# Performance work log

Measured on AMD Instinct MI355X. Metric: run time of the kernel, lower is better.

The kernel has to match this reference:

```python
import jax, jax.numpy as jnp
import numpy as np

J = 25
C_IN, HID, LAT = 3, 64, 32


def _graph_conv(x, A, W, b):
    # x: [N,T,J,Cin]; A: [J,J]; W: [Cin,Cout]; b: [Cout]
    A = jax.nn.softmax(A, axis=-1)
    # fused adjacency mix + projection: (A @ x) @ W + b
    x = jnp.einsum('ij,ntjc->ntic', A, x)
    return jnp.einsum('ntjc,cd->ntjd', x, W) + b


def setup_inputs() -> dict:
    key = jax.random.key(0)
    ks = jax.random.split(key, 13)
    x = jax.random.normal(ks[0], (32, 2048, J, C_IN), dtype=jnp.float32)
    eye = jnp.eye(J, dtype=jnp.float32)
    def lin(kw, kb, cin, cout):
        W = jax.random.normal(kw, (cin, cout), dtype=jnp.float32) / np.sqrt(cin)
        b = jax.random.normal(kb, (cout,), dtype=jnp.float32) * 0.01
        return W, b
    W1, b1 = lin(ks[1], ks[2], C_IN, HID)
    W2, b2 = lin(ks[3], ks[4], HID, LAT)
    W3, b3 = lin(ks[5], ks[6], LAT, HID)
    W4, b4 = lin(ks[7], ks[8], HID, C_IN)
    return {
        'x': x,
        'A1': eye, 'W1': W1, 'b1': b1,
        'A2': eye, 'W2': W2, 'b2': b2,
        'A3': eye, 'W3': W3, 'b3': b3,
        'A4': eye, 'W4': W4, 'b4': b4,
    }


def reference(x, A1, W1, b1, A2, W2, b2, A3, W3, b3, A4, W4, b4):
    h = jax.nn.relu(_graph_conv(x, A1, W1, b1))     # encoder_g1 + relu
    z = _graph_conv(h, A2, W2, b2)                  # encoder_g2 (no relu)
    h_dec = jax.nn.relu(_graph_conv(z, A3, W3, b3)) # decoder_g1 + relu
    out = _graph_conv(h_dec, A4, W4, b4)            # decoder_g2
    return out
```

## Files before the change

kernel.cpp:

```cpp
#include <hip/hip_runtime.h>
#include <math.h>

#define J 25
#define NJC 75
#define NWAVE 4
#define NTHREADS 256
#define NFPW 16

#define O_A1P  0
#define O_APP  1024
#define O_A4B  2048
#define O_W2T  3072
#define O_W3T  5120
#define O_W1A  7168
#define O_W4C  8192
#define O_B4   8512
#define O_BPPF 8576
#define CWS_SZ 8704

using bf16x2 = __attribute__((ext_vector_type(2))) __bf16;
using bf16x8 = __attribute__((ext_vector_type(8))) __bf16;
using f32x4  = __attribute__((ext_vector_type(4))) float;
using f32x16 = __attribute__((ext_vector_type(16))) float;

__device__ inline bf16x8 zero8() {
    bf16x8 z;
    #pragma unroll
    for (int j = 0; j < 8; j++) z[j] = (__bf16)0.f;
    return z;
}

#if defined(__has_builtin)
#if __has_builtin(__builtin_amdgcn_cvt_pk_bf16_f32)
#define HAVE_PK_BF16 1
#endif
#endif

__device__ inline bf16x2 cvt2(float a, float b) {
#ifdef HAVE_PK_BF16
    return __builtin_amdgcn_cvt_pk_bf16_f32(a, b);
#else
    bf16x2 r; r[0] = (__bf16)a; r[1] = (__bf16)b; return r;
#endif
}
__device__ inline bf16x8 pk8(const f32x16& acc, int st) {
    const int b = 8 * st;
    bf16x8 r;
    #pragma unroll
    for (int p = 0; p < 4; p++) {
        bf16x2 v = cvt2(acc[b + 2 * p], acc[b + 2 * p + 1]);
        r[2 * p] = v[0]; r[2 * p + 1] = v[1];
    }
    return r;
}

__global__ __launch_bounds__(NTHREADS, 2) void gcn_fused(
    const float* __restrict__ x,
    const float* __restrict__ A1, const float* __restrict__ W1, const float* __restrict__ b1,
    const float* __restrict__ A2, const float* __restrict__ W2, const float* __restrict__ b2,
    const float* __restrict__ A3, const float* __restrict__ W3, const float* __restrict__ b3,
    const float* __restrict__ A4, const float* __restrict__ W4, const float* __restrict__ b4,
    float* __restrict__ out)
{
    __shared__ __align__(16) float  TS[3189];
    __shared__ __align__(16) __bf16 CWS[CWS_SZ];

    const int t = threadIdx.x;

    {
        float* T   = TS;
        float* bpp = T + 3125;
        float* T0 = T;        float* T1 = T + 625;  float* T2 = T + 1250;
        float* T3 = T + 1875; float* T4 = T + 2500;

        if (t < 100) {
            const int m = t / J, i = t % J;
            const float* Asrc = (m == 0) ? A1 : (m == 1) ? A2 : (m == 2) ? A3 : A4;
            float row[J];
            float mx = -1e30f;
            #pragma unroll
            for (int j = 0; j < J; j++) { row[j] = Asrc[i * J + j]; mx = fmaxf(mx, row[j]); }
            float s = 0.f;
            #pragma unroll
            for (int j = 0; j < J; j++) { row[j] = __expf(row[j] - mx); s += row[j]; }
            const float inv = 1.f / s;
            float* dst = T + m * 625 + i * J;
            #pragma unroll
            for (int j = 0; j < J; j++) dst[j] = row[j] * inv;
        }
        if (t < 64) {
            float s = b3[t];
            #pragma unroll
            for (int l = 0; l < 32; l++) s += W3[l * 64 + t] * b2[l];
            bpp[t] = s;
        }
        __syncthreads();

        for (int idx = t; idx < 625; idx += 256) {
            const int i = idx / J, jj = idx % J;
            float s = 0.f;
            #pragma unroll
            for (int k = 0; k < J; k++) s += T2[i * J + k] * T1[k * J + jj];
            T4[idx] = s;
        }
        __syncthreads();

        for (int i = t; i < 1024; i += 256) {
            const int b = i >> 8, n = (i >> 3) & 31, jj = i & 7;
            const int s = b >> 1, h = b & 1, r = 8 * s + jj;
            const int k32 = (r & 3) + 8 * (r >> 2) + 4 * h;
            const bool ok = (k32 < J && n < J);
            CWS[O_A1P + i] = (__bf16)(ok ? T0[n * J + k32] : 0.f);
            CWS[O_APP + i] = (__bf16)(ok ? T4[n * J + k32] : 0.f);
            CWS[O_A4B + i] = (__bf16)(ok ? T3[n * J + k32] : 0.f);
        }
        for (int i = t; i < 2048; i += 256) {
            {
                const int b = i >> 8, n = (i >> 3) & 31, jj = i & 7;
                const int s = b >> 1, h = b & 1, r = 8 * (s & 1) + jj;
                const int d = 32 * (s >> 1) + (r & 3) + 8 * (r >> 2) + 4 * h;
                CWS[O_W2T + i] = (__bf16)W2[d * 32 + n];
            }
            {
                const int tt = i >> 10, rr = i & 1023;
                const int b = rr >> 8, m = (rr >> 3) & 31, jj = rr & 7;
                const int s = b >> 1, h = b & 1, r = 8 * s + jj;
                const int l = (r & 3) + 8 * (r >> 2) + 4 * h;
                CWS[O_W3T + i] = (__bf16)W3[l * 64 + tt * 32 + m];
            }
        }
        for (int i = t; i < 1024; i += 256) {
            const int tile = i >> 9, rr = i & 511, hf_ = rr >> 8, n = (rr >> 3) & 31, jj = rr & 7;
            const int k = 8 * hf_ + jj;
            const int d = tile * 32 + n;
            float v = 0.f;
            if (k < 3) v = W1[k * 64 + d];
            else if (k == 3) v = b1[d];
            CWS[O_W1A + i] = (__bf16)v;
        }
        {
            const int c = t >> 6, b = (t >> 3) & 7, jj = t & 7;
            const int s = b >> 1, h = b & 1, r = 8 * (s & 1) + jj;
            const int d = 32 * (s >> 1) + (r & 3) + 8 * (r >> 2) + 4 * h;
            CWS[O_W4C + t] = (c < 3) ? (__bf16)W4[d * 3 + c] : (__bf16)0.f;
        }
        {
            float* fwB = (float*)(CWS + O_BPPF);
            if (t < 64) {
                const int g = t >> 4, h = (t >> 3) & 1, jj = t & 7;
                const int tt = g >> 1, st = g & 1;
                const int row32 = (jj & 3) + 16 * st + 8 * (jj >> 2) + 4 * h;
                fwB[t] = bpp[tt * 32 + row32];
            }
            float* fb4 = (float*)(CWS + O_B4);
            if (t >= 64 && t < 68) fb4[t - 64] = (t < 67) ? b4[t - 64] : 0.f;
        }
        __syncthreads();
    }

    const int w = t >> 6, lane = t & 63, ln = lane & 31, half = lane >> 5;
    const int fo = ln * 8;

    const long fbase = ((long)blockIdx.x * NWAVE + w) * NFPW;

    const float* xp = x + fbase * NJC;
    float* op = out + fbase * NJC;

    const bool xact = (lane < J);
    const int xoff = lane * 3;

    float xr[2][3];
    #pragma unroll
    for (int u = 0; u < 2; u++) { xr[u][0] = xr[u][1] = xr[u][2] = 0.f; }
    if (xact) {
        const float* q = xp + xoff;
        xr[0][0] = q[0]; xr[0][1] = q[1]; xr[0][2] = q[2];
    }
    xp += NJC;
    if (NFPW > 1) {
        if (xact) {
            const float* q = xp + xoff;
            xr[1][0] = q[0]; xr[1][1] = q[1]; xr[1][2] = q[2];
        }
        xp += NJC;
    }

    bf16x8 rA1P[2], rApp[2], rA4b[2], rW1A[2], rW2[4], rW3[4], rW4[4];
    #pragma unroll
    for (int ks = 0; ks < 2; ks++) {
        rA1P[ks] = *(const bf16x8*)&CWS[O_A1P + (2 * ks + half) * 256 + fo];
        rApp[ks] = *(const bf16x8*)&CWS[O_APP + (2 * ks + half) * 256 + fo];
        rA4b[ks] = *(const bf16x8*)&CWS[O_A4B + (2 * ks + half) * 256 + fo];
        rW1A[ks] = *(const bf16x8*)&CWS[O_W1A + ks * 512 + half * 256 + fo];
    }
    #pragma unroll
    for (int ks = 0; ks < 4; ks++)
        rW2[ks] = *(const bf16x8*)&CWS[O_W2T + (half + 2 * ks) * 256 + fo];
    #pragma unroll
    for (int tt = 0; tt < 2; tt++)
        #pragma unroll
        for (int ks = 0; ks < 2; ks++)
            rW3[tt * 2 + ks] = *(const bf16x8*)&CWS[O_W3T + tt * 1024 + (half + 2 * ks) * 256 + fo];
    #pragma unroll
    for (int ks = 0; ks < 4; ks++) {
        rW4[ks] = zero8();
        if (ln < 3) rW4[ks] = *(const bf16x8*)&CWS[O_W4C + ln * 64 + (half + 2 * ks) * 8];
    }
    f32x16 rB16[2];
    {
        const float* fwB = (const float*)(CWS + O_BPPF);
        #pragma unroll
        for (int tt = 0; tt < 2; tt++)
            #pragma unroll
            for (int st = 0; st < 2; st++) {
                f32x4 qa = *(const f32x4*)&fwB[32 * tt + 16 * st + 8 * half + 0];
                f32x4 qb = *(const f32x4*)&fwB[32 * tt + 16 * st + 8 * half + 4];
                #pragma unroll
                for (int j = 0; j < 4; j++) {
                    rB16[tt][8 * st + j]     = qa[j];
                    rB16[tt][8 * st + 4 + j] = qb[j];
                }
            }
    }
    const float* fb4 = (const float*)(CWS + O_B4);
    const float b40 = fb4[0], b41 = fb4[1], b42 = fb4[2];

    f32x16 Z;
    #pragma unroll
    for (int z = 0; z < 16; z++) Z[z] = 0.f;

    const bool do_store = (lane < J);

    #pragma unroll
    for (int fi = 0; fi < NFPW; fi++) {
        const int cur = fi & 1;

        bf16x8 xa = zero8();
        if (xact) {
            xa[0] = (__bf16)xr[cur][0];
            xa[1] = (__bf16)xr[cur][1];
            xa[2] = (__bf16)xr[cur][2];
            xa[3] = (__bf16)1.f;
        }
        if (fi + 2 < NFPW) {
            if (xact) {
                const float* q = xp + xoff;
                xr[cur][0] = q[0]; xr[cur][1] = q[1]; xr[cur][2] = q[2];
            }
            xp += NJC;
        }

        f32x16 accG0 = __builtin_amdgcn_mfma_f32_32x32x16_bf16(xa, rW1A[0], Z, 0, 0, 0);
        f32x16 accG1 = __builtin_amdgcn_mfma_f32_32x32x16_bf16(xa, rW1A[1], Z, 0, 0, 0);
        bf16x8 ga0 = pk8(accG0, 0), ga1 = pk8(accG0, 1);
        bf16x8 ga2 = pk8(accG1, 0), ga3 = pk8(accG1, 1);

        bf16x8 hf[4];
        {
            f32x16 accH0 = __builtin_amdgcn_mfma_f32_32x32x16_bf16(ga0, rA1P[0], Z, 0, 0, 0);
            accH0 = __builtin_amdgcn_mfma_f32_32x32x16_bf16(ga1, rA1P[1], accH0, 0, 0, 0);
            f32x16 accH1 = __builtin_amdgcn_mfma_f32_32x32x16_bf16(ga2, rA1P[0], Z, 0, 0, 0);
            accH1 = __builtin_amdgcn_mfma_f32_32x32x16_bf16(ga3, rA1P[1], accH1, 0, 0, 0);
            #pragma unroll
            for (int z = 0; z < 16; z++) {
                accH0[z] = fmaxf(accH0[z], 0.f);
                accH1[z] = fmaxf(accH1[z], 0.f);
            }
            hf[0] = pk8(accH0, 0); hf[1] = pk8(accH0, 1);
            hf[2] = pk8(accH1, 0); hf[3] = pk8(accH1, 1);
        }

        f32x16 accU = __builtin_amdgcn_mfma_f32_32x32x16_bf16(hf[0], rW2[0], Z, 0, 0, 0);
        #pragma unroll
        for (int s = 1; s < 4; s++)
            accU = __builtin_amdgcn_mfma_f32_32x32x16_bf16(hf[s], rW2[s], accU, 0, 0, 0);
        bf16x8 uf[2] = { pk8(accU, 0), pk8(accU, 1) };

        f32x16 accV = __builtin_amdgcn_mfma_f32_32x32x16_bf16(uf[0], rApp[0], Z, 0, 0, 0);
        accV = __builtin_amdgcn_mfma_f32_32x32x16_bf16(uf[1], rApp[1], accV, 0, 0, 0);
        bf16x8 vf[2] = { pk8(accV, 0), pk8(accV, 1) };

        bf16x8 hd[4];
        #pragma unroll
        for (int tt = 0; tt < 2; tt++) {
            f32x16 acc = __builtin_amdgcn_mfma_f32_32x32x16_bf16(rW3[tt * 2 + 0], vf[0], rB16[tt], 0, 0, 0);
            acc = __builtin_amdgcn_mfma_f32_32x32x16_bf16(rW3[tt * 2 + 1], vf[1], acc, 0, 0, 0);
            #pragma unroll
            for (int z = 0; z < 16; z++) acc[z] = fmaxf(acc[z], 0.f);
            hd[2 * tt]     = pk8(acc, 0);
            hd[2 * tt + 1] = pk8(acc, 1);
        }

        f32x16 accP = __builtin_amdgcn_mfma_f32_32x32x16_bf16(hd[0], rW4[0], Z, 0, 0, 0);
        #pragma unroll
        for (int s = 1; s < 4; s++)
            accP = __builtin_amdgcn_mfma_f32_32x32x16_bf16(hd[s], rW4[s], accP, 0, 0, 0);
        bf16x8 pf[2] = { pk8(accP, 0), pk8(accP, 1) };

        f32x16 accO = __builtin_amdgcn_mfma_f32_32x32x16_bf16(pf[0], rA4b[0], Z, 0, 0, 0);
        accO = __builtin_amdgcn_mfma_f32_32x32x16_bf16(pf[1], rA4b[1], accO, 0, 0, 0);
        if (do_store) {
            op[lane * 3 + 0] = accO[0] + b40;
            op[lane * 3 + 1] = accO[1] + b41;
            op[lane * 3 + 2] = accO[2] + b42;
        }
        op += NJC;
    }
}

extern "C" void kernel_launch(void* const* d_in, const int* in_sizes, int n_in,
                              void* d_out, int out_size, void* d_ws, size_t ws_size,
                              hipStream_t stream)
{
    const float* x  = (const float*)d_in[0];
    const float* A1 = (const float*)d_in[1];
    const float* W1 = (const float*)d_in[2];
    const float* b1 = (const float*)d_in[3];
    const float* A2 = (const float*)d_in[4];
    const float* W2 = (const float*)d_in[5];
    const float* b2 = (const float*)d_in[6];
    const float* A3 = (const float*)d_in[7];
    const float* W3 = (const float*)d_in[8];
    const float* b3 = (const float*)d_in[9];
    const float* A4 = (const float*)d_in[10];
    const float* W4 = (const float*)d_in[11];
    const float* b4 = (const float*)d_in[12];
    float* out = (float*)d_out;
    (void)d_ws; (void)ws_size;

    const int NT = in_sizes[0] / NJC;
    const int nblocks = NT / (NWAVE * NFPW);

    gcn_fused<<<nblocks, NTHREADS, 0, stream>>>(
        x, A1, W1, b1, A2, W2, b2, A3, W3, b3, A4, W4, b4, out);
}
```

Baseline: 145.2 us.

## Software-pipeline frame loop, interleaving encoder and decoder MFMA chains across frames

```diff
diff --git a/kernel.cpp b/kernel.cpp
--- a/kernel.cpp
+++ b/kernel.cpp
@@ -5,7 +5,7 @@
 #define NJC 75
 #define NWAVE 4
 #define NTHREADS 256
-#define NFPW 16
+#define NFPW 32
 
 #define O_A1P  0
 #define O_APP  1024
@@ -169,21 +169,12 @@
     const bool xact = (lane < J);
     const int xoff = lane * 3;
 
-    float xr[2][3];
-    #pragma unroll
-    for (int u = 0; u < 2; u++) { xr[u][0] = xr[u][1] = xr[u][2] = 0.f; }
+    float xc0 = 0.f, xc1 = 0.f, xc2 = 0.f;
     if (xact) {
         const float* q = xp + xoff;
-        xr[0][0] = q[0]; xr[0][1] = q[1]; xr[0][2] = q[2];
+        xc0 = q[0]; xc1 = q[1]; xc2 = q[2];
     }
     xp += NJC;
-    if (NFPW > 1) {
-        if (xact) {
-            const float* q = xp + xoff;
-            xr[1][0] = q[0]; xr[1][1] = q[1]; xr[1][2] = q[2];
-        }
-        xp += NJC;
-    }
 
     bf16x8 rA1P[2], rApp[2], rA4b[2], rW1A[2], rW2[4], rW3[4], rW4[4];
     #pragma unroll
@@ -231,80 +222,148 @@
 
     const bool do_store = (lane < J);
 
-    #pragma unroll
-    for (int fi = 0; fi < NFPW; fi++) {
-        const int cur = fi & 1;
-
+    bf16x8 ufP0, ufP1;
+
+    {
         bf16x8 xa = zero8();
         if (xact) {
-            xa[0] = (__bf16)xr[cur][0];
-            xa[1] = (__bf16)xr[cur][1];
-            xa[2] = (__bf16)xr[cur][2];
-            xa[3] = (__bf16)1.f;
-        }
-        if (fi + 2 < NFPW) {
-            if (xact) {
-                const float* q = xp + xoff;
-                xr[cur][0] = q[0]; xr[cur][1] = q[1]; xr[cur][2] = q[2];
-            }
-            xp += NJC;
-        }
+            xa[0] = (__bf16)xc0; xa[1] = (__bf16)xc1;
+            xa[2] = (__bf16)xc2; xa[3] = (__bf16)1.f;
+        }
+        if (xact) {
+            const float* q = xp + xoff;
+            xc0 = q[0]; xc1 = q[1]; xc2 = q[2];
+        }
+        xp += NJC;
 
         f32x16 accG0 = __builtin_amdgcn_mfma_f32_32x32x16_bf16(xa, rW1A[0], Z, 0, 0, 0);
         f32x16 accG1 = __builtin_amdgcn_mfma_f32_32x32x16_bf16(xa, rW1A[1], Z, 0, 0, 0);
         bf16x8 ga0 = pk8(accG0, 0), ga1 = pk8(accG0, 1);
         bf16x8 ga2 = pk8(accG1, 0), ga3 = pk8(accG1, 1);
 
-        bf16x8 hf[4];
-        {
-            f32x16 accH0 = __builtin_amdgcn_mfma_f32_32x32x16_bf16(ga0, rA1P[0], Z, 0, 0, 0);
-            accH0 = __builtin_amdgcn_mfma_f32_32x32x16_bf16(ga1, rA1P[1], accH0, 0, 0, 0);
-            f32x16 accH1 = __builtin_amdgcn_mfma_f32_32x32x16_bf16(ga2, rA1P[0], Z, 0, 0, 0);
-            accH1 = __builtin_amdgcn_mfma_f32_32x32x16_bf16(ga3, rA1P[1], accH1, 0, 0, 0);
-            #pragma unroll
-            for (int z = 0; z < 16; z++) {
-                accH0[z] = fmaxf(accH0[z], 0.f);
-                accH1[z] = fmaxf(accH1[z], 0.f);
-            }
-            hf[0] = pk8(accH0, 0); hf[1] = pk8(accH0, 1);
-            hf[2] = pk8(accH1, 0); hf[3] = pk8(accH1, 1);
-        }
-
-        f32x16 accU = __builtin_amdgcn_mfma_f32_32x32x16_bf16(hf[0], rW2[0], Z, 0, 0, 0);
-        #pragma unroll
-        for (int s = 1; s < 4; s++)
-            accU = __builtin_amdgcn_mfma_f32_32x32x16_bf16(hf[s], rW2[s], accU, 0, 0, 0);
-        bf16x8 uf[2] = { pk8(accU, 0), pk8(accU, 1) };
-
-        f32x16 accV = __builtin_amdgcn_mfma_f32_32x32x16_bf16(uf[0], rApp[0], Z, 0, 0, 0);
-        accV = __builtin_amdgcn_mfma_f32_32x32x16_bf16(uf[1], rApp[1], accV, 0, 0, 0);
-        bf16x8 vf[2] = { pk8(accV, 0), pk8(accV, 1) };
-
-        bf16x8 hd[4];
-        #pragma unroll
-        for (int tt = 0; tt < 2; tt++) {
-            f32x16 acc = __builtin_amdgcn_mfma_f32_32x32x16_bf16(rW3[tt * 2 + 0], vf[0], rB16[tt], 0, 0, 0);
-            acc = __builtin_amdgcn_mfma_f32_32x32x16_bf16(rW3[tt * 2 + 1], vf[1], acc, 0, 0, 0);
-            #pragma unroll
-            for (int z = 0; z < 16; z++) acc[z] = fmaxf(acc[z], 0.f);
-            hd[2 * tt]     = pk8(acc, 0);
-            hd[2 * tt + 1] = pk8(acc, 1);
-        }
-
-        f32x16 accP = __builtin_amdgcn_mfma_f32_32x32x16_bf16(hd[0], rW4[0], Z, 0, 0, 0);
-        #pragma unroll
-        for (int s = 1; s < 4; s++)
-            accP = __builtin_amdgcn_mfma_f32_32x32x16_bf16(hd[s], rW4[s], accP, 0, 0, 0);
-        bf16x8 pf[2] = { pk8(accP, 0), pk8(accP, 1) };
-
-        f32x16 accO = __builtin_amdgcn_mfma_f32_32x32x16_bf16(pf[0], rA4b[0], Z, 0, 0, 0);
-        accO = __builtin_amdgcn_mfma_f32_32x32x16_bf16(pf[1], rA4b[1], accO, 0, 0, 0);
+        f32x16 accH0 = __builtin_amdgcn_mfma_f32_32x32x16_bf16(ga0, rA1P[0], Z, 0, 0, 0);
+        accH0 = __builtin_amdgcn_mfma_f32_32x32x16_bf16(ga1, rA1P[1], accH0, 0, 0, 0);
+        f32x16 accH1 = __builtin_amdgcn_mfma_f32_32x32x16_bf16(ga2, rA1P[0], Z, 0, 0, 0);
+        accH1 = __builtin_amdgcn_mfma_f32_32x32x16_bf16(ga3, rA1P[1], accH1, 0, 0, 0);
+        #pragma unroll
+        for (int z = 0; z < 16; z++) {
+            accH0[z] = fmaxf(accH0[z], 0.f);
+            accH1[z] = fmaxf(accH1[z], 0.f);
+        }
+        bf16x8 hf0 = pk8(accH0, 0), hf1 = pk8(accH0, 1);
+        bf16x8 hf2 = pk8(accH1, 0), hf3 = pk8(accH1, 1);
+
+        f32x16 accU = __builtin_amdgcn_mfma_f32_32x32x16_bf16(hf0, rW2[0], Z, 0, 0, 0);
+        accU = __builtin_amdgcn_mfma_f32_32x32x16_bf16(hf1, rW2[1], accU, 0, 0, 0);
+        accU = __builtin_amdgcn_mfma_f32_32x32x16_bf16(hf2, rW2[2], accU, 0, 0, 0);
+        accU = __builtin_amdgcn_mfma_f32_32x32x16_bf16(hf3, rW2[3], accU, 0, 0, 0);
+        ufP0 = pk8(accU, 0); ufP1 = pk8(accU, 1);
+    }
+
+    #pragma unroll 1
+    for (int fi = 1; fi < NFPW; fi++) {
+        bf16x8 xa = zero8();
+        if (xact) {
+            xa[0] = (__bf16)xc0; xa[1] = (__bf16)xc1;
+            xa[2] = (__bf16)xc2; xa[3] = (__bf16)1.f;
+        }
+        if (fi + 1 < NFPW && xact) {
+            const float* q = xp + xoff;
+            xc0 = q[0]; xc1 = q[1]; xc2 = q[2];
+        }
+        xp += NJC;
+
+        f32x16 accV = __builtin_amdgcn_mfma_f32_32x32x16_bf16(ufP0, rApp[0], Z, 0, 0, 0);
+        f32x16 accG0 = __builtin_amdgcn_mfma_f32_32x32x16_bf16(xa, rW1A[0], Z, 0, 0, 0);
+        accV = __builtin_amdgcn_mfma_f32_32x32x16_bf16(ufP1, rApp[1], accV, 0, 0, 0);
+        f32x16 accG1 = __builtin_amdgcn_mfma_f32_32x32x16_bf16(xa, rW1A[1], Z, 0, 0, 0);
+
+        bf16x8 vf0 = pk8(accV, 0), vf1 = pk8(accV, 1);
+
+        f32x16 acc50 = __builtin_amdgcn_mfma_f32_32x32x16_bf16(rW3[0], vf0, rB16[0], 0, 0, 0);
+        f32x16 acc51 = __builtin_amdgcn_mfma_f32_32x32x16_bf16(rW3[2], vf0, rB16[1], 0, 0, 0);
+        acc50 = __builtin_amdgcn_mfma_f32_32x32x16_bf16(rW3[1], vf1, acc50, 0, 0, 0);
+        acc51 = __builtin_amdgcn_mfma_f32_32x32x16_bf16(rW3[3], vf1, acc51, 0, 0, 0);
+
+        bf16x8 ga0 = pk8(accG0, 0), ga1 = pk8(accG0, 1);
+        bf16x8 ga2 = pk8(accG1, 0), ga3 = pk8(accG1, 1);
+
+        f32x16 accH0 = __builtin_amdgcn_mfma_f32_32x32x16_bf16(ga0, rA1P[0], Z, 0, 0, 0);
+        accH0 = __builtin_amdgcn_mfma_f32_32x32x16_bf16(ga1, rA1P[1], accH0, 0, 0, 0);
+        f32x16 accH1 = __builtin_amdgcn_mfma_f32_32x32x16_bf16(ga2, rA1P[0], Z, 0, 0, 0);
+        accH1 = __builtin_amdgcn_mfma_f32_32x32x16_bf16(ga3, rA1P[1], accH1, 0, 0, 0);
+
+        #pragma unroll
+        for (int z = 0; z < 16; z++) {
+            acc50[z] = fmaxf(acc50[z], 0.f);
+            acc51[z] = fmaxf(acc51[z], 0.f);
+        }
+        bf16x8 hd0 = pk8(acc50, 0), hd1 = pk8(acc50, 1);
+        bf16x8 hd2 = pk8(acc51, 0), hd3 = pk8(acc51, 1);
+
+        f32x16 accP = __builtin_amdgcn_mfma_f32_32x32x16_bf16(hd0, rW4[0], Z, 0, 0, 0);
+        accP = __builtin_amdgcn_mfma_f32_32x32x16_bf16(hd1, rW4[1], accP, 0, 0, 0);
+        accP = __builtin_amdgcn_mfma_f32_32x32x16_bf16(hd2, rW4[2], accP, 0, 0, 0);
+        accP = __builtin_amdgcn_mfma_f32_32x32x16_bf16(hd3, rW4[3], accP, 0, 0, 0);
+
+        #pragma unroll
+        for (int z = 0; z < 16; z++) {
+            accH0[z] = fmaxf(accH0[z], 0.f);
+            accH1[z] = fmaxf(accH1[z], 0.f);
+        }
+        bf16x8 hf0 = pk8(accH0, 0), hf1 = pk8(accH0, 1);
+        bf16x8 hf2 = pk8(accH1, 0), hf3 = pk8(accH1, 1);
+
+        f32x16 accU = __builtin_amdgcn_mfma_f32_32x32x16_bf16(hf0, rW2[0], Z, 0, 0, 0);
+        accU = __builtin_amdgcn_mfma_f32_32x32x16_bf16(hf1, rW2[1], accU, 0, 0, 0);
+        accU = __builtin_amdgcn_mfma_f32_32x32x16_bf16(hf2, rW2[2], accU, 0, 0, 0);
+        accU = __builtin_amdgcn_mfma_f32_32x32x16_bf16(hf3, rW2[3], accU, 0, 0, 0);
+
+        bf16x8 pf0 = pk8(accP, 0), pf1 = pk8(accP, 1);
+
+        f32x16 accO = __builtin_amdgcn_mfma_f32_32x32x16_bf16(pf0, rA4b[0], Z, 0, 0, 0);
+        accO = __builtin_amdgcn_mfma_f32_32x32x16_bf16(pf1, rA4b[1], accO, 0, 0, 0);
+
+        ufP0 = pk8(accU, 0); ufP1 = pk8(accU, 1);
+
         if (do_store) {
             op[lane * 3 + 0] = accO[0] + b40;
             op[lane * 3 + 1] = accO[1] + b41;
             op[lane * 3 + 2] = accO[2] + b42;
         }
         op += NJC;
+    }
+
+    {
+        f32x16 accV = __builtin_amdgcn_mfma_f32_32x32x16_bf16(ufP0, rApp[0], Z, 0, 0, 0);
+        accV = __builtin_amdgcn_mfma_f32_32x32x16_bf16(ufP1, rApp[1], accV, 0, 0, 0);
+        bf16x8 vf0 = pk8(accV, 0), vf1 = pk8(accV, 1);
+
+        f32x16 acc50 = __builtin_amdgcn_mfma_f32_32x32x16_bf16(rW3[0], vf0, rB16[0], 0, 0, 0);
+        acc50 = __builtin_amdgcn_mfma_f32_32x32x16_bf16(rW3[1], vf1, acc50, 0, 0, 0);
+        f32x16 acc51 = __builtin_amdgcn_mfma_f32_32x32x16_bf16(rW3[2], vf0, rB16[1], 0, 0, 0);
+        acc51 = __builtin_amdgcn_mfma_f32_32x32x16_bf16(rW3[3], vf1, acc51, 0, 0, 0);
+        #pragma unroll
+        for (int z = 0; z < 16; z++) {
+            acc50[z] = fmaxf(acc50[z], 0.f);
+            acc51[z] = fmaxf(acc51[z], 0.f);
+        }
+        bf16x8 hd0 = pk8(acc50, 0), hd1 = pk8(acc50, 1);
+        bf16x8 hd2 = pk8(acc51, 0), hd3 = pk8(acc51, 1);
+
+        f32x16 accP = __builtin_amdgcn_mfma_f32_32x32x16_bf16(hd0, rW4[0], Z, 0, 0, 0);
+        accP = __builtin_amdgcn_mfma_f32_32x32x16_bf16(hd1, rW4[1], accP, 0, 0, 0);
+        accP = __builtin_amdgcn_mfma_f32_32x32x16_bf16(hd2, rW4[2], accP, 0, 0, 0);
+        accP = __builtin_amdgcn_mfma_f32_32x32x16_bf16(hd3, rW4[3], accP, 0, 0, 0);
+        bf16x8 pf0 = pk8(accP, 0), pf1 = pk8(accP, 1);
+
+        f32x16 accO = __builtin_amdgcn_mfma_f32_32x32x16_bf16(pf0, rA4b[0], Z, 0, 0, 0);
+        accO = __builtin_amdgcn_mfma_f32_32x32x16_bf16(pf1, rA4b[1], accO, 0, 0, 0);
+        if (do_store) {
+            op[lane * 3 + 0] = accO[0] + b40;
+            op[lane * 3 + 1] = accO[1] + b41;
+            op[lane * 3 + 2] = accO[2] + b42;
+        }
     }
 }
 
```

After: 138.4 us. 4.7% less time.
